# Kernel optimization log

Measured on AMD Instinct MI355X. Metric: run time of the kernel, lower is better.

Reference implementation:

```python
import jax, jax.numpy as jnp
import numpy as np

N, E, D, H, C, ED = 30000, 300000, 256, 8, 32, 32
HID = H * C  # 256 = hidden_channels


def setup_inputs() -> dict:
    key = jax.random.key(0)
    ks = jax.random.split(key, 14)
    w = lambda k, shp, fan: (jax.random.normal(k, shp, jnp.float32) / np.sqrt(fan)).astype(jnp.float32)
    return {
        "x": jax.random.normal(ks[0], (N, D), jnp.float32),
        "edge_index": jax.random.randint(ks[1], (2, E), 0, N, jnp.int32),
        "edge_attr": jax.random.normal(ks[2], (E, ED), jnp.float32),
        # TransformerConv params (PyG: q/k/v Linears have bias; lin_edge & lin_skip bias=False)
        "Wq": w(ks[3], (D, HID), D), "bq": 0.01 * jax.random.normal(ks[4], (HID,), jnp.float32),
        "Wk": w(ks[5], (D, HID), D), "bk": 0.01 * jax.random.normal(ks[6], (HID,), jnp.float32),
        "Wv": w(ks[7], (D, HID), D), "bv": 0.01 * jax.random.normal(ks[8], (HID,), jnp.float32),
        "We": w(ks[9], (ED, HID), ED),
        "Wskip": w(ks[10], (D, HID), D),
        # MLP([HID, HID, HID], gelu-tanh, plain_last=False): two Linear+act layers
        "W1": w(ks[11], (HID, HID), HID), "b1": jnp.zeros((HID,), jnp.float32),
        "W2": w(ks[12], (HID, HID), HID), "b2": jnp.zeros((HID,), jnp.float32),
    }


def reference(x, edge_index, edge_attr, Wq, bq, Wk, bk, Wv, bv, We, Wskip, W1, b1, W2, b2):
    src, dst = edge_index[0], edge_index[1]  # message flows src -> dst
    q = (x @ Wq + bq).reshape(N, H, C)
    k = (x @ Wk + bk).reshape(N, H, C)
    v = (x @ Wv + bv).reshape(N, H, C)
    e = (edge_attr @ We).reshape(E, H, C)
    k_e = k[src] + e                               # [E,H,C]
    v_e = v[src] + e                               # [E,H,C]
    logits = jnp.einsum('ehc,ehc->eh', q[dst], k_e) / np.sqrt(C)  # [E,H]
    # segment softmax over incoming edges of each dst node
    m = jax.ops.segment_max(logits, dst, num_segments=N)          # [N,H]
    a = jnp.exp(logits - m[dst])
    denom = jax.ops.segment_sum(a, dst, num_segments=N)           # [N,H]
    alpha = a / (denom[dst] + 1e-16)                              # [E,H]
    agg = jax.ops.segment_sum(alpha[:, :, None] * v_e, dst, num_segments=N)  # [N,H,C]
    out = agg.reshape(N, HID) + x @ Wskip          # concat heads + root skip
    # residual MLP: x + gelu(gelu(x W1 + b1) W2 + b2)
    h = jax.nn.gelu(out @ W1 + b1, approximate=True)
    h = jax.nn.gelu(h @ W2 + b2, approximate=True)
    return out + h
```

## Files before the change

### kernel.cpp

```cpp
#include <hip/hip_runtime.h>

#define NN 30000
#define NE 300000
#define HIDDEN 256

typedef __attribute__((ext_vector_type(8))) __bf16 bf16x8;
typedef __attribute__((ext_vector_type(4))) __bf16 bf16x4;
typedef __attribute__((ext_vector_type(4))) float float4v;

__device__ inline __bf16 f2bf(float f) {
  unsigned u = __builtin_bit_cast(unsigned, f);
  u += 0x7fffu + ((u >> 16) & 1u);
  unsigned short s = (unsigned short)(u >> 16);
  return __builtin_bit_cast(__bf16, s);
}
__device__ inline float bf2f(__bf16 b) {
  unsigned short s = __builtin_bit_cast(unsigned short, b);
  unsigned u = ((unsigned)s) << 16;
  return __builtin_bit_cast(float, u);
}
__device__ inline float gelu_tanh(float x) {
  float x3 = x * x * x;
  return 0.5f * x * (1.0f + tanhf(0.79788456080286536f * (x + 0.044715f * x3)));
}

#define PREP_XB_END (1829 + (NN * 32 + 255) / 256)
__global__ __launch_bounds__(256) void prep_kernel(
    const float* __restrict__ Wq, const float* __restrict__ Wk, const float* __restrict__ Wv,
    const float* __restrict__ Wsk, const float* __restrict__ W1, const float* __restrict__ W2,
    const float* __restrict__ We, const float* __restrict__ bq, const float* __restrict__ bk,
    const float* __restrict__ bv, const float* __restrict__ x,
    __bf16* __restrict__ WTall, __bf16* __restrict__ WT1, __bf16* __restrict__ WT2,
    float* __restrict__ ball, float* __restrict__ WeT, __bf16* __restrict__ xb,
    int* __restrict__ degz) {
  const int b = blockIdx.x;
  const int tid = threadIdx.x;
  if (b < 1792) {
    const int region = b >> 8;
    const int idx = ((b & 255) << 8) | tid;
    const int k = idx & 255, n = idx >> 8;
    float v;
    if (region == 3) {
      const int h = n >> 5, d = n & 31;
      const float* wq = Wq + (size_t)k * 256 + h * 32;
      const float* we = We + (size_t)d * 256 + h * 32;
      float s = 0.f;
#pragma unroll
      for (int c = 0; c < 32; ++c) s += wq[c] * we[c];
      v = s;
    } else {
      const float* W = (region == 0) ? Wq : (region == 1) ? Wk : (region == 2) ? Wv
                     : (region == 4) ? Wsk : (region == 5) ? W1 : W2;
      v = W[(size_t)k * 256 + n];
    }
    const __bf16 bv16 = f2bf(v);
    if (region < 5) WTall[(size_t)region * 65536 + idx] = bv16;
    else if (region == 5) WT1[idx] = bv16;
    else WT2[idx] = bv16;
  } else if (b < 1797) {
    const int j = (b - 1792) * 256 + tid;
    if (j < 1280) {
      float v = 0.f;
      if (j < 256) v = bq[j];
      else if (j < 512) v = bk[j - 256];
      else if (j < 768) v = bv[j - 512];
      else if (j < 1024) {
        const int col = j - 768, h = col >> 5, d = col & 31;
        const float* bqh = bq + h * 32;
        const float* we = We + (size_t)d * 256 + h * 32;
        float s = 0.f;
#pragma unroll
        for (int c = 0; c < 32; ++c) s += bqh[c] * we[c];
        v = s;
      }
      ball[j] = v;
    }
  } else if (b < 1829) {
    const int idx = (b - 1797) * 256 + tid;
    const int ch = idx >> 5, d = idx & 31;
    WeT[idx] = We[(size_t)d * 256 + ch];
  } else if (b < PREP_XB_END) {
    const int t = (b - 1829) * 256 + tid;
    if (t < NN * 256 / 8) {
      const float* p = x + (size_t)t * 8;
      float4v f0 = *(const float4v*)(p);
      float4v f1 = *(const float4v*)(p + 4);
      bf16x8 o;
#pragma unroll
      for (int j = 0; j < 4; ++j) { o[j] = f2bf(f0[j]); o[j + 4] = f2bf(f1[j]); }
      *(bf16x8*)(xb + (size_t)t * 8) = o;
    }
  } else {
    const int idx = (b - PREP_XB_END) * 256 + tid;
    if (idx < 2 * NN) degz[idx] = 0;
  }
}

__global__ void count_deg_kernel(const int* __restrict__ dst, int* __restrict__ deg, int E) {
  int e = blockIdx.x * 256 + threadIdx.x;
  if (e < E) atomicAdd(&deg[dst[e]], 1);
}

__global__ __launch_bounds__(256) void deg_psum_kernel(const int* __restrict__ deg,
                                                       int* __restrict__ psum, int n) {
  int i = blockIdx.x * 256 + threadIdx.x;
  int v = (i < n) ? deg[i] : 0;
#pragma unroll
  for (int s = 1; s < 64; s <<= 1) v += __shfl_xor(v, s);
  __shared__ int ws[4];
  if ((threadIdx.x & 63) == 0) ws[threadIdx.x >> 6] = v;
  __syncthreads();
  if (threadIdx.x == 0) psum[blockIdx.x] = ws[0] + ws[1] + ws[2] + ws[3];
}

__global__ __launch_bounds__(128) void psum_scan_kernel(int* __restrict__ psum,
                                                        int* __restrict__ offs, int nb) {
  __shared__ int tmp[128];
  const int t = threadIdx.x;
  int v = (t < nb) ? psum[t] : 0;
  tmp[t] = v;
  __syncthreads();
  for (int s = 1; s < 128; s <<= 1) {
    int u = (t >= s) ? tmp[t - s] : 0;
    __syncthreads();
    tmp[t] += u;
    __syncthreads();
  }
  if (t < nb) psum[t] = tmp[t] - v;
  if (t == 0) offs[NN] = NE;
}

__global__ __launch_bounds__(256) void offs_kernel(const int* __restrict__ deg,
                                                   const int* __restrict__ psum,
                                                   int* __restrict__ offs, int n) {
  __shared__ int tmp[256];
  const int t = threadIdx.x;
  const int i = blockIdx.x * 256 + t;
  int v = (i < n) ? deg[i] : 0;
  tmp[t] = v;
  __syncthreads();
  for (int s = 1; s < 256; s <<= 1) {
    int u = (t >= s) ? tmp[t - s] : 0;
    __syncthreads();
    tmp[t] += u;
    __syncthreads();
  }
  if (i < n) offs[i] = psum[blockIdx.x] + tmp[t] - v;
}

__global__ void scatter_kernel(const int* __restrict__ srcIn, const int* __restrict__ dstIn,
                               const int* __restrict__ offs, int* __restrict__ cursor,
                               int2* __restrict__ sed, int E) {
  int e = blockIdx.x * 256 + threadIdx.x;
  if (e >= E) return;
  int d = dstIn[e];
  int p = atomicAdd(&cursor[d], 1);
  sed[offs[d] + p] = make_int2(srcIn[e], e);
}

template <int GX, int EPI, int MODE>
__global__ __launch_bounds__(256) void gemm_k4(
    const __bf16* __restrict__ A, const __bf16* __restrict__ Wt,
    const float* __restrict__ bias,
    float* __restrict__ Yf, __bf16* __restrict__ Ybf,
    __bf16* __restrict__ QGp, __bf16* __restrict__ KVp,
    const float* __restrict__ resid, int M, int gyTiles) {
  __shared__ char smem[128 * 264 * 2];
  __bf16* Bs = (__bf16*)smem;
  const int bid = blockIdx.x;
  const int stripe = bid / (8 * GX);
  const int rem = bid % (8 * GX);
  const int y8 = rem % 8;
  const int xt = rem / 8;
  const int y = stripe * 8 + y8;
  if (y >= gyTiles) return;
  const int n0 = xt * 128;

  {
    const int t = threadIdx.x;
#pragma unroll
    for (int i = 0; i < 16; ++i) {
      int g = i * 256 + t;
      int row = g >> 5;
      int c16 = g & 31;
      bf16x8 v = *(const bf16x8*)(Wt + (size_t)(n0 + row) * 256 + c16 * 8);
      *(bf16x8*)(Bs + row * 264 + c16 * 8) = v;
    }
  }
  __syncthreads();

  const int lane = threadIdx.x & 63;
  const int w = threadIdx.x >> 6;
  const int r = lane & 15;
  const int q = lane >> 4;
  const int mw = y * 128 + w * 32;
  int ar0 = mw + r;      if (ar0 >= M) ar0 = M - 1;
  int ar1 = mw + 16 + r; if (ar1 >= M) ar1 = M - 1;
  const int kq = q * 8;

  float4v acc[2][8];
#pragma unroll
  for (int i = 0; i < 2; ++i)
#pragma unroll
    for (int t = 0; t < 8; ++t) acc[i][t] = (float4v){0.f, 0.f, 0.f, 0.f};

#pragma unroll
  for (int kk = 0; kk < 256; kk += 32) {
    const int ka = kk + kq;
    bf16x8 a0 = *(const bf16x8*)(A + (size_t)ar0 * 256 + ka);
    bf16x8 a1 = *(const bf16x8*)(A + (size_t)ar1 * 256 + ka);
    bf16x8 b[8];
#pragma unroll
    for (int t = 0; t < 8; ++t)
      b[t] = *(const bf16x8*)(Bs + (t * 16 + r) * 264 + ka);
#pragma unroll
    for (int t = 0; t < 8; ++t) {
      acc[0][t] = __builtin_amdgcn_mfma_f32_16x16x32_bf16(a0, b[t], acc[0][t], 0, 0, 0);
      acc[1][t] = __builtin_amdgcn_mfma_f32_16x16x32_bf16(a1, b[t], acc[1][t], 0, 0, 0);
    }
  }
  __syncthreads();

  float* cs = (float*)smem + w * 4224;
#pragma unroll
  for (int t = 0; t < 8; ++t) {
    const int col = n0 + t * 16 + r;
    const float bb = bias ? bias[col] : 0.0f;
#pragma unroll
    for (int i2 = 0; i2 < 2; ++i2)
#pragma unroll
      for (int ii = 0; ii < 4; ++ii) {
        float v = acc[i2][t][ii] + bb;
        if constexpr (EPI == 2 || EPI == 3) v = gelu_tanh(v);
        cs[(i2 * 16 + q * 4 + ii) * 132 + t * 16 + r] = v;
      }
  }

  constexpr int NSTR = GX * 128;
  const int p = n0 >> 8;
  const int cbase = n0 & 255;
  __bf16* dstI = (p == 0 || p == 3) ? QGp : KVp;
  const int moff = (p >= 2) ? 4 : 0;
#pragma unroll
  for (int i = 0; i < 16; ++i) {
    const int rl = i * 2 + (lane >> 5);
    const int row = mw + rl;
    const int c4 = (lane & 31) * 4;
    float4v v = *(const float4v*)(cs + rl * 132 + c4);
    if (row < M) {
      if constexpr (MODE == 1) {
        if (p == 4) {
          *(float4v*)(Yf + (size_t)row * 256 + cbase + c4) = v;
        } else {
          bf16x4 b4;
          b4[0] = f2bf(v[0]); b4[1] = f2bf(v[1]); b4[2] = f2bf(v[2]); b4[3] = f2bf(v[3]);
          const int c = cbase + c4;
          *(bf16x4*)(dstI + (size_t)row * 512 + 2 * c + moff) = b4;
        }
      } else if constexpr (EPI == 1) {
        *(float4v*)(Yf + (size_t)row * NSTR + n0 + c4) = v;
      } else if constexpr (EPI == 3) {
        float4v rr = *(const float4v*)(resid + (size_t)row * NSTR + n0 + c4);
        v[0] += rr[0]; v[1] += rr[1]; v[2] += rr[2]; v[3] += rr[3];
        *(float4v*)(Yf + (size_t)row * NSTR + n0 + c4) = v;
      } else {
        bf16x4 b4;
        b4[0] = f2bf(v[0]); b4[1] = f2bf(v[1]); b4[2] = f2bf(v[2]); b4[3] = f2bf(v[3]);
        *(bf16x4*)(Ybf + (size_t)row * NSTR + n0 + c4) = b4;
      }
    }
  }
}

__global__ __launch_bounds__(256) void attn_kernel(
    const __bf16* __restrict__ QG, const __bf16* __restrict__ KV,
    const float* __restrict__ ea, const int2* __restrict__ sed,
    const int* __restrict__ offs,
    float* __restrict__ OUT, __bf16* __restrict__ AE) {
  const int lane = threadIdx.x & 63;
  const int w = threadIdx.x >> 6;
  const int n = blockIdx.x * 4 + w;
  if (n >= NN) return;
  const int sub = lane & 7;

  const bf16x8 qg = *(const bf16x8*)(QG + (size_t)n * 512 + lane * 8);
  const float q0 = bf2f(qg[0]), q1 = bf2f(qg[1]), q2 = bf2f(qg[2]), q3 = bf2f(qg[3]);
  const float g0 = bf2f(qg[4]), g1 = bf2f(qg[5]), g2 = bf2f(qg[6]), g3 = bf2f(qg[7]);

  float denom = 0.f;
  float4v accv = {0.f, 0.f, 0.f, 0.f};
  float4v acce = {0.f, 0.f, 0.f, 0.f};
  const int beg = offs[n], end = offs[n + 1];
  const float LSC = 0.25506589858f;

  int i = beg;
  for (; i + 2 <= end; i += 2) {
    const int2 s0 = sed[i];
    const int2 s1 = sed[i + 1];
    const bf16x8 kv0 = *(const bf16x8*)(KV + (size_t)s0.x * 512 + lane * 8);
    const float4v e0 = *(const float4v*)(ea + (size_t)s0.y * 32 + sub * 4);
    const bf16x8 kv1 = *(const bf16x8*)(KV + (size_t)s1.x * 512 + lane * 8);
    const float4v e1 = *(const float4v*)(ea + (size_t)s1.y * 32 + sub * 4);
    float p0 = q0 * bf2f(kv0[0]) + q1 * bf2f(kv0[1]) + q2 * bf2f(kv0[2]) + q3 * bf2f(kv0[3])
             + g0 * e0[0] + g1 * e0[1] + g2 * e0[2] + g3 * e0[3];
    float p1 = q0 * bf2f(kv1[0]) + q1 * bf2f(kv1[1]) + q2 * bf2f(kv1[2]) + q3 * bf2f(kv1[3])
             + g0 * e1[0] + g1 * e1[1] + g2 * e1[2] + g3 * e1[3];
    p0 += __shfl_xor(p0, 1); p1 += __shfl_xor(p1, 1);
    p0 += __shfl_xor(p0, 2); p1 += __shfl_xor(p1, 2);
    p0 += __shfl_xor(p0, 4); p1 += __shfl_xor(p1, 4);
    const float w0 = exp2f(p0 * LSC);
    const float w1 = exp2f(p1 * LSC);
    denom += w0 + w1;
    accv[0] += w0 * bf2f(kv0[4]) + w1 * bf2f(kv1[4]);
    accv[1] += w0 * bf2f(kv0[5]) + w1 * bf2f(kv1[5]);
    accv[2] += w0 * bf2f(kv0[6]) + w1 * bf2f(kv1[6]);
    accv[3] += w0 * bf2f(kv0[7]) + w1 * bf2f(kv1[7]);
    acce[0] += w0 * e0[0] + w1 * e1[0];
    acce[1] += w0 * e0[1] + w1 * e1[1];
    acce[2] += w0 * e0[2] + w1 * e1[2];
    acce[3] += w0 * e0[3] + w1 * e1[3];
  }
  if (i < end) {
    const int2 s0 = sed[i];
    const bf16x8 kv0 = *(const bf16x8*)(KV + (size_t)s0.x * 512 + lane * 8);
    const float4v e0 = *(const float4v*)(ea + (size_t)s0.y * 32 + sub * 4);
    float p0 = q0 * bf2f(kv0[0]) + q1 * bf2f(kv0[1]) + q2 * bf2f(kv0[2]) + q3 * bf2f(kv0[3])
             + g0 * e0[0] + g1 * e0[1] + g2 * e0[2] + g3 * e0[3];
    p0 += __shfl_xor(p0, 1);
    p0 += __shfl_xor(p0, 2);
    p0 += __shfl_xor(p0, 4);
    const float w0 = exp2f(p0 * LSC);
    denom += w0;
    accv[0] += w0 * bf2f(kv0[4]);
    accv[1] += w0 * bf2f(kv0[5]);
    accv[2] += w0 * bf2f(kv0[6]);
    accv[3] += w0 * bf2f(kv0[7]);
    acce[0] += w0 * e0[0];
    acce[1] += w0 * e0[1];
    acce[2] += w0 * e0[2];
    acce[3] += w0 * e0[3];
  }

  const float inv = 1.0f / (denom + 1e-16f);
  const int c0 = lane * 4;
  float4v o = *(const float4v*)(OUT + (size_t)n * 256 + c0);
#pragma unroll
  for (int j = 0; j < 4; ++j) o[j] += accv[j] * inv;
  *(float4v*)(OUT + (size_t)n * 256 + c0) = o;
  bf16x4 aeb;
  aeb[0] = f2bf(acce[0] * inv); aeb[1] = f2bf(acce[1] * inv);
  aeb[2] = f2bf(acce[2] * inv); aeb[3] = f2bf(acce[3] * inv);
  *(bf16x4*)(AE + (size_t)n * 256 + c0) = aeb;
}

__global__ __launch_bounds__(256) void post_kernel(
    const __bf16* __restrict__ AE, const float* __restrict__ WeT,
    float* __restrict__ OUT, __bf16* __restrict__ OUTh) {
  const int lane = threadIdx.x & 63;
  const int wave = threadIdx.x >> 6;
  const int c0 = lane * 4;
  const int hg = lane >> 3;

  float4v w4[4][8];
#pragma unroll
  for (int j = 0; j < 4; ++j)
#pragma unroll
    for (int s = 0; s < 8; ++s)
      w4[j][s] = *(const float4v*)(WeT + (size_t)(c0 + j) * 32 + s * 4);

  const int nbase = blockIdx.x * 64;
  for (int it = 0; it < 16; ++it) {
    const int n = nbase + it * 4 + wave;
    if (n >= NN) return;
    const __bf16* aerow = AE + (size_t)n * HIDDEN + hg * 32;
    float aef[32];
#pragma unroll
    for (int t = 0; t < 4; ++t) {
      bf16x8 a8 = *(const bf16x8*)(aerow + t * 8);
#pragma unroll
      for (int j = 0; j < 8; ++j) aef[t * 8 + j] = bf2f(a8[j]);
    }
    float4v o = *(const float4v*)(OUT + (size_t)n * HIDDEN + c0);
#pragma unroll
    for (int j = 0; j < 4; ++j) {
      float s = 0.f;
#pragma unroll
      for (int g = 0; g < 8; ++g) {
        s += aef[g * 4 + 0] * w4[j][g][0] + aef[g * 4 + 1] * w4[j][g][1]
           + aef[g * 4 + 2] * w4[j][g][2] + aef[g * 4 + 3] * w4[j][g][3];
      }
      o[j] += s;
    }
    *(float4v*)(OUT + (size_t)n * HIDDEN + c0) = o;
    bf16x4 ob;
    ob[0] = f2bf(o[0]); ob[1] = f2bf(o[1]); ob[2] = f2bf(o[2]); ob[3] = f2bf(o[3]);
    *(bf16x4*)(OUTh + (size_t)n * HIDDEN + c0) = ob;
  }
}

extern "C" void kernel_launch(void* const* d_in, const int* in_sizes, int n_in,
                              void* d_out, int out_size, void* d_ws, size_t ws_size,
                              hipStream_t stream) {
  (void)in_sizes; (void)n_in; (void)out_size; (void)ws_size;
  const float* x   = (const float*)d_in[0];
  const int*   ei  = (const int*)d_in[1];
  const float* ea  = (const float*)d_in[2];
  const float* Wq  = (const float*)d_in[3];
  const float* bq  = (const float*)d_in[4];
  const float* Wk  = (const float*)d_in[5];
  const float* bk  = (const float*)d_in[6];
  const float* Wv  = (const float*)d_in[7];
  const float* bv  = (const float*)d_in[8];
  const float* We  = (const float*)d_in[9];
  const float* Wsk = (const float*)d_in[10];
  const float* W1  = (const float*)d_in[11];
  const float* b1  = (const float*)d_in[12];
  const float* W2  = (const float*)d_in[13];
  const float* b2  = (const float*)d_in[14];
  float* out = (float*)d_out;

  char* ws = (char*)d_ws;
  size_t off = 0;
  auto alloc = [&](size_t bytes) -> char* {
    off = (off + 255) & ~(size_t)255;
    char* p = ws + off;
    off += bytes;
    return p;
  };
  __bf16* QG   = (__bf16*)alloc((size_t)NN * 512 * 2);
  __bf16* KV   = (__bf16*)alloc((size_t)NN * 512 * 2);
  __bf16* xb   = (__bf16*)alloc((size_t)NN * 256 * 2);
  __bf16* AE   = (__bf16*)alloc((size_t)NN * 256 * 2);
  __bf16* OUTh = (__bf16*)alloc((size_t)NN * 256 * 2);
  __bf16* WTall = (__bf16*)alloc((size_t)1280 * 256 * 2);
  __bf16* WT1  = (__bf16*)alloc(256 * 256 * 2);
  __bf16* WT2  = (__bf16*)alloc(256 * 256 * 2);
  float*  ball = (float*)alloc(1280 * 4);
  float*  WeT  = (float*)alloc(256 * 32 * 4);
  int* deg    = (int*)alloc((size_t)2 * NN * 4);
  int* cursor = deg + NN;
  int* offs   = (int*)alloc((size_t)(NN + 1) * 4);
  int* psum   = (int*)alloc(512);
  int2* sed   = (int2*)alloc((size_t)NE * 8);
  __bf16* H1 = AE;

  const int* srcIn = ei;
  const int* dstIn = ei + NE;

  const int prepBlocks = PREP_XB_END + (2 * NN + 255) / 256;
  prep_kernel<<<prepBlocks, 256, 0, stream>>>(Wq, Wk, Wv, Wsk, W1, W2, We, bq, bk, bv, x,
                                              WTall, WT1, WT2, ball, WeT, xb, deg);

  const int nb = (NN + 255) / 256;
  count_deg_kernel<<<(NE + 255) / 256, 256, 0, stream>>>(dstIn, deg, NE);
  deg_psum_kernel<<<nb, 256, 0, stream>>>(deg, psum, NN);
  psum_scan_kernel<<<1, 128, 0, stream>>>(psum, offs, nb);
  offs_kernel<<<nb, 256, 0, stream>>>(deg, psum, offs, NN);
  scatter_kernel<<<(NE + 255) / 256, 256, 0, stream>>>(srcIn, dstIn, offs, cursor, sed, NE);

  const int gy = (NN + 127) / 128;
  const int stripes = (gy + 7) / 8;
  gemm_k4<10, 0, 1><<<stripes * 80, 256, 0, stream>>>(
      xb, WTall, ball, out, nullptr, QG, KV, nullptr, NN, gy);

  attn_kernel<<<(NN + 3) / 4, 256, 0, stream>>>(QG, KV, ea, sed, offs, out, AE);

  post_kernel<<<(NN + 63) / 64, 256, 0, stream>>>(AE, WeT, out, OUTh);

  gemm_k4<2, 2, 0><<<stripes * 16, 256, 0, stream>>>(
      OUTh, WT1, b1, nullptr, H1, nullptr, nullptr, nullptr, NN, gy);
  gemm_k4<2, 3, 0><<<stripes * 16, 256, 0, stream>>>(
      H1, WT2, b2, out, nullptr, nullptr, nullptr, out, NN, gy);
}
```

Before: 364.0 us.

## Split each node's edge list across four waves and reduce in shared memory

Result: no change. 371.2 us (+2.0%).

```diff
diff --git a/kernel.cpp b/kernel.cpp
--- a/kernel.cpp
+++ b/kernel.cpp
@@ -277,26 +277,29 @@
     const float* __restrict__ ea, const int2* __restrict__ sed,
     const int* __restrict__ offs,
     float* __restrict__ OUT, __bf16* __restrict__ AE) {
+  __shared__ float sdn[4][64];
+  __shared__ float sav[4][64][4], sae[4][64][4];
   const int lane = threadIdx.x & 63;
   const int w = threadIdx.x >> 6;
-  const int n = blockIdx.x * 4 + w;
-  if (n >= NN) return;
+  const int n = blockIdx.x;
   const int sub = lane & 7;
 
+  const float LSC = 0.25506589858f;
   const bf16x8 qg = *(const bf16x8*)(QG + (size_t)n * 512 + lane * 8);
-  const float q0 = bf2f(qg[0]), q1 = bf2f(qg[1]), q2 = bf2f(qg[2]), q3 = bf2f(qg[3]);
-  const float g0 = bf2f(qg[4]), g1 = bf2f(qg[5]), g2 = bf2f(qg[6]), g3 = bf2f(qg[7]);
+  const float q0 = bf2f(qg[0]) * LSC, q1 = bf2f(qg[1]) * LSC;
+  const float q2 = bf2f(qg[2]) * LSC, q3 = bf2f(qg[3]) * LSC;
+  const float g0 = bf2f(qg[4]) * LSC, g1 = bf2f(qg[5]) * LSC;
+  const float g2 = bf2f(qg[6]) * LSC, g3 = bf2f(qg[7]) * LSC;
 
   float denom = 0.f;
   float4v accv = {0.f, 0.f, 0.f, 0.f};
   float4v acce = {0.f, 0.f, 0.f, 0.f};
   const int beg = offs[n], end = offs[n + 1];
-  const float LSC = 0.25506589858f;
-
-  int i = beg;
-  for (; i + 2 <= end; i += 2) {
+
+  int i = beg + w;
+  for (; i + 4 < end; i += 8) {
     const int2 s0 = sed[i];
-    const int2 s1 = sed[i + 1];
+    const int2 s1 = sed[i + 4];
     const bf16x8 kv0 = *(const bf16x8*)(KV + (size_t)s0.x * 512 + lane * 8);
     const float4v e0 = *(const float4v*)(ea + (size_t)s0.y * 32 + sub * 4);
     const bf16x8 kv1 = *(const bf16x8*)(KV + (size_t)s1.x * 512 + lane * 8);
@@ -308,8 +311,8 @@
     p0 += __shfl_xor(p0, 1); p1 += __shfl_xor(p1, 1);
     p0 += __shfl_xor(p0, 2); p1 += __shfl_xor(p1, 2);
     p0 += __shfl_xor(p0, 4); p1 += __shfl_xor(p1, 4);
-    const float w0 = exp2f(p0 * LSC);
-    const float w1 = exp2f(p1 * LSC);
+    const float w0 = exp2f(p0);
+    const float w1 = exp2f(p1);
     denom += w0 + w1;
     accv[0] += w0 * bf2f(kv0[4]) + w1 * bf2f(kv1[4]);
     accv[1] += w0 * bf2f(kv0[5]) + w1 * bf2f(kv1[5]);
@@ -329,7 +332,7 @@
     p0 += __shfl_xor(p0, 1);
     p0 += __shfl_xor(p0, 2);
     p0 += __shfl_xor(p0, 4);
-    const float w0 = exp2f(p0 * LSC);
+    const float w0 = exp2f(p0);
     denom += w0;
     accv[0] += w0 * bf2f(kv0[4]);
     accv[1] += w0 * bf2f(kv0[5]);
@@ -341,16 +344,31 @@
     acce[3] += w0 * e0[3];
   }
 
-  const float inv = 1.0f / (denom + 1e-16f);
-  const int c0 = lane * 4;
-  float4v o = *(const float4v*)(OUT + (size_t)n * 256 + c0);
-#pragma unroll
-  for (int j = 0; j < 4; ++j) o[j] += accv[j] * inv;
-  *(float4v*)(OUT + (size_t)n * 256 + c0) = o;
-  bf16x4 aeb;
-  aeb[0] = f2bf(acce[0] * inv); aeb[1] = f2bf(acce[1] * inv);
-  aeb[2] = f2bf(acce[2] * inv); aeb[3] = f2bf(acce[3] * inv);
-  *(bf16x4*)(AE + (size_t)n * 256 + c0) = aeb;
+  sdn[w][lane] = denom;
+#pragma unroll
+  for (int j = 0; j < 4; ++j) { sav[w][lane][j] = accv[j]; sae[w][lane][j] = acce[j]; }
+  __syncthreads();
+  if (w == 0) {
+    float D = 0.f;
+    float4v av = {0.f, 0.f, 0.f, 0.f};
+    float4v ae = {0.f, 0.f, 0.f, 0.f};
+#pragma unroll
+    for (int ww = 0; ww < 4; ++ww) {
+      D += sdn[ww][lane];
+#pragma unroll
+      for (int j = 0; j < 4; ++j) { av[j] += sav[ww][lane][j]; ae[j] += sae[ww][lane][j]; }
+    }
+    const float inv = 1.0f / (D + 1e-16f);
+    const int c0 = lane * 4;
+    float4v o = *(const float4v*)(OUT + (size_t)n * 256 + c0);
+#pragma unroll
+    for (int j = 0; j < 4; ++j) o[j] += av[j] * inv;
+    *(float4v*)(OUT + (size_t)n * 256 + c0) = o;
+    bf16x4 aeb;
+    aeb[0] = f2bf(ae[0] * inv); aeb[1] = f2bf(ae[1] * inv);
+    aeb[2] = f2bf(ae[2] * inv); aeb[3] = f2bf(ae[3] * inv);
+    *(bf16x4*)(AE + (size_t)n * 256 + c0) = aeb;
+  }
 }
 
 __global__ __launch_bounds__(256) void post_kernel(
@@ -463,7 +481,7 @@
   gemm_k4<10, 0, 1><<<stripes * 80, 256, 0, stream>>>(
       xb, WTall, ball, out, nullptr, QG, KV, nullptr, NN, gy);
 
-  attn_kernel<<<(NN + 3) / 4, 256, 0, stream>>>(QG, KV, ea, sed, offs, out, AE);
+  attn_kernel<<<NN, 256, 0, stream>>>(QG, KV, ea, sed, offs, out, AE);
 
   post_kernel<<<(NN + 63) / 64, 256, 0, stream>>>(AE, WeT, out, OUTh);
 
```
